# Performance work log

Measured on AMD Instinct MI355X. Metric: run time of the kernel, lower is better.

The kernel has to match this reference:

```python
import jax, jax.numpy as jnp
import numpy as np

HEADS = 8
HIDDEN = 512
SEQ = 1024
BATCH = 8
SCALE = 1.2
TOPK = round(0.05 * SEQ)  # 51, as in mode='stocastic'


def setup_inputs() -> dict:
    key = jax.random.key(0)
    ks = jax.random.split(key, 12)
    d = HIDDEN
    s = 0.02
    return {
        "Query_x": jax.random.normal(ks[0], (BATCH, SEQ, d), jnp.float32),
        "KeyandValue_x": jax.random.normal(ks[1], (BATCH, SEQ, d), jnp.float32),
        "Wq": jax.random.normal(ks[2], (d, d), jnp.float32) * s,
        "bq": jnp.zeros((d,), jnp.float32),
        "Wk": jax.random.normal(ks[3], (d, d), jnp.float32) * s,
        "bk": jnp.zeros((d,), jnp.float32),
        "Wv": jax.random.normal(ks[4], (d, d), jnp.float32) * s,
        "bv": jnp.zeros((d,), jnp.float32),
        "Wo": jax.random.normal(ks[5], (d, d), jnp.float32) * s,
        "bo": jnp.zeros((d,), jnp.float32),
        "randidx": jax.random.randint(ks[6], (round(0.1 * SEQ),), 0, SEQ, jnp.int32),
    }


def _split_heads(x, B, S):
    # torch: split last dim into heads chunks, cat along dim 0 -> [heads*B, S, dk]
    dk = HIDDEN // HEADS
    return x.reshape(B, S, HEADS, dk).transpose(2, 0, 1, 3).reshape(HEADS * B, S, dk)


def _merge_heads(x, B, S):
    dk = HIDDEN // HEADS
    return x.reshape(HEADS, B, S, dk).transpose(1, 2, 0, 3).reshape(B, S, HIDDEN)


def moderate_attention(a, randidx):
    # a: [N, S, L] softmaxed attention. Scale top-k + random columns by SCALE,
    # then renormalize rows. torch scatter_ writes a*SCALE gathered from the
    # pre-scatter tensor, so duplicate indices are idempotent -> boolean mask.
    N, S, L = a.shape
    _, idx = jax.lax.top_k(a, TOPK)                       # [N, S, k]
    rand_b = jnp.broadcast_to(randidx.astype(idx.dtype), (N, S, randidx.shape[0]))
    all_idx = jnp.concatenate([idx, rand_b], axis=-1)      # [N, S, k+r]
    n_ix = jnp.arange(N)[:, None, None]
    q_ix = jnp.arange(S)[None, :, None]
    sel = jnp.zeros(a.shape, bool).at[n_ix, q_ix, all_idx].set(True)
    a2 = jnp.where(sel, a * SCALE, a)
    return a2 / jnp.sum(a2, axis=-1, keepdims=True)


def reference(Query_x, KeyandValue_x, Wq, bq, Wk, bk, Wv, bv, Wo, bo, randidx):
    B, S, _ = Query_x.shape
    dk = HIDDEN // HEADS
    Q = _split_heads(Query_x @ Wq + bq, B, S)          # [H*B, S, dk]
    K = _split_heads(KeyandValue_x @ Wk + bk, B, S)
    V = _split_heads(KeyandValue_x @ Wv + bv, B, S)
    scores = jnp.einsum('nqd,nkd->nqk', Q, K) / jnp.sqrt(jnp.float32(dk))
    a = jax.nn.softmax(scores, axis=-1)
    a = moderate_attention(a, randidx)
    out = jnp.einsum('nqk,nkd->nqd', a, V)
    return _merge_heads(out, B, S) @ Wo + bo
```

## Files before the change

kernel.cpp:

```cpp
#include <hip/hip_runtime.h>
#include <stdint.h>

typedef unsigned short ushort_t;
typedef __bf16 bf16x8 __attribute__((ext_vector_type(8)));
typedef _Float16 f16x8v __attribute__((ext_vector_type(8)));
typedef __fp16 fp16x2 __attribute__((ext_vector_type(2)));
typedef float f32x4 __attribute__((ext_vector_type(4)));

#define SEQ   1024
#define DK    64
#define TOPK_N 51
#define RSCALE 1.2f

#define OFF_WT  0
#define OFF_Q   (4*512*512)
#define OFF_K   (OFF_Q  + 64*1024*64)
#define OFF_V   (OFF_K  + 64*1024*64)
#define OFF_QX  (OFF_V  + 64*1024*64)
#define OFF_KVX (OFF_QX + 8192*512)
#define OFF_MASK (OFF_KVX + 8192*512)
#define OFF_A   OFF_QX

static __device__ __forceinline__ ushort_t f2bf(float f){
  union { float f; unsigned u; } x; x.f = f;
  unsigned r = x.u + 0x7FFFu + ((x.u >> 16) & 1u);
  return (ushort_t)(r >> 16);
}
static __device__ __forceinline__ ushort_t f2h(float f){
  union { _Float16 h; ushort_t u; } x; x.h = (_Float16)f; return x.u;
}
static __device__ __forceinline__ float h2f(ushort_t u){
  union { ushort_t u; _Float16 h; } x; x.u = u; return (float)x.h;
}
static __device__ __forceinline__ unsigned pk2(float a, float b){
  union { fp16x2 h; unsigned u; } x;
  x.h = __builtin_amdgcn_cvt_pkrtz(a, b);
  return x.u;
}
static __device__ __forceinline__ bf16x8 frag16(const ushort_t* p){
  union { uint4 u; bf16x8 b; } x; x.u = *(const uint4*)p; return x.b;
}
static __device__ __forceinline__ f16x8v frag16h(const ushort_t* p){
  union { uint4 u; f16x8v h; } x; x.u = *(const uint4*)p; return x.h;
}
static __device__ __forceinline__ void gll16(const ushort_t* g, ushort_t* lds){
  __builtin_amdgcn_global_load_lds((const __attribute__((address_space(1))) unsigned*)g,
                                   (__attribute__((address_space(3))) unsigned*)lds,
                                   16, 0, 0);
}

__global__ __launch_bounds__(256) void prep_k(const float* qx, const float* kvx,
    const float* Wq, const float* Wk, const float* Wv, const float* Wo,
    const int* ridx, int nrand, ushort_t* ws){
  __shared__ ushort_t t[64][72];
  __shared__ unsigned wds[64];
  int bid = blockIdx.x, tid = threadIdx.x;

  if (bid < 4096){
    const float* src = (bid >= 2048) ? kvx : qx;
    ushort_t* dst = ws + ((bid >= 2048) ? OFF_KVX : OFF_QX);
    int i = ((bid & 2047)*256 + tid) * 8;
    float4 a = *(const float4*)(src + i);
    float4 b = *(const float4*)(src + i + 4);
    union { ushort_t s[8]; uint4 u; } p;
    p.s[0]=f2bf(a.x); p.s[1]=f2bf(a.y); p.s[2]=f2bf(a.z); p.s[3]=f2bf(a.w);
    p.s[4]=f2bf(b.x); p.s[5]=f2bf(b.y); p.s[6]=f2bf(b.z); p.s[7]=f2bf(b.w);
    *(uint4*)(dst + i) = p.u;
  } else if (bid < 4352){
    int rb = bid - 4096;
    int z = rb >> 6, rem = rb & 63;
    const float* W = z==0?Wq: z==1?Wk: z==2?Wv: Wo;
    ushort_t* O = ws + OFF_WT + (size_t)z*512*512;
    int kt = (rem >> 3)*64, nt = (rem & 7)*64;
    int r0 = tid>>3, c8 = (tid&7)*8;
    #pragma unroll
    for (int p=0;p<2;p++){
      int r = p*32 + r0;
      float4 a = *(const float4*)&W[(size_t)(kt+r)*512 + nt + c8];
      float4 b = *(const float4*)&W[(size_t)(kt+r)*512 + nt + c8 + 4];
      t[r][c8+0]=f2bf(a.x); t[r][c8+1]=f2bf(a.y); t[r][c8+2]=f2bf(a.z); t[r][c8+3]=f2bf(a.w);
      t[r][c8+4]=f2bf(b.x); t[r][c8+5]=f2bf(b.y); t[r][c8+6]=f2bf(b.z); t[r][c8+7]=f2bf(b.w);
    }
    __syncthreads();
    #pragma unroll
    for (int p=0;p<2;p++){
      int r = p*32 + r0;
      union { ushort_t s[8]; uint4 u; } tmp;
      #pragma unroll
      for (int j=0;j<8;j++) tmp.s[j] = t[c8+j][r];
      *(uint4*)&O[(size_t)(nt+r)*512 + kt + c8] = tmp.u;
    }
  } else {
    if (tid < 64) wds[tid] = 0;
    __syncthreads();
    for (int i = tid; i < nrand; i += 256){
      int col = ridx[i];
      atomicOr(&wds[(col >> 3) & 63], 1u << (((col >> 9) << 3) | (col & 7)));
    }
    __syncthreads();
    if (tid < 64) (ws + OFF_MASK)[tid] = (ushort_t)wds[tid];
  }
}

__global__ __launch_bounds__(256) void gemm_k(ushort_t* ws, const float* bq, const float* bk,
    const float* bv, const float* bo, float* dout, int base_mode){
  int mode = base_mode + blockIdx.z;
  const ushort_t* X  = (mode==0)? ws+OFF_QX : (mode==3)? ws+OFF_A : ws+OFF_KVX;
  const ushort_t* WT = ws + OFF_WT + (size_t)mode*(512*512);
  const float* bias  = (mode==0)?bq:(mode==1)?bk:(mode==2)?bv:bo;
  ushort_t* out = (mode==0)? ws+OFF_Q : (mode==1)? ws+OFF_K : ws+OFF_V;

  __shared__ ushort_t sA[128*64];
  __shared__ ushort_t sB[128*64];
  int tid = threadIdx.x, lane = tid & 63, w = tid >> 6;
  int wm = w & 1, wn = w >> 1;
  int m0 = blockIdx.y * 128, n0 = blockIdx.x * 128;
  int r16 = lane & 15, quad = lane >> 4;
  int srow = lane >> 3, schunk = lane & 7;

  const f32x4 zero = {0.f,0.f,0.f,0.f};
  f32x4 acc[4][4];
  #pragma unroll
  for (int i=0;i<4;i++)
    #pragma unroll
    for (int j=0;j<4;j++) acc[i][j] = zero;

  for (int kb = 0; kb < 8; kb++){
    int k0 = kb*64;
    #pragma unroll
    for (int i=0;i<4;i++){
      int rb = w*32 + i*8;
      int gch = schunk ^ srow;
      gll16(X  + (size_t)(m0+rb+srow)*512 + k0 + gch*8, sA + rb*64);
      gll16(WT + (size_t)(n0+rb+srow)*512 + k0 + gch*8, sB + rb*64);
    }
    __syncthreads();
    #pragma unroll
    for (int t=0;t<2;t++){
      bf16x8 aF[4], bF[4];
      #pragma unroll
      for (int i=0;i<4;i++){
        int row = wm*64 + i*16 + r16;
        aF[i] = frag16(sA + row*64 + ((t*4 + quad) ^ (row & 7))*8);
      }
      #pragma unroll
      for (int j=0;j<4;j++){
        int row = wn*64 + j*16 + r16;
        bF[j] = frag16(sB + row*64 + ((t*4 + quad) ^ (row & 7))*8);
      }
      #pragma unroll
      for (int i=0;i<4;i++)
        #pragma unroll
        for (int j=0;j<4;j++)
          acc[i][j] = __builtin_amdgcn_mfma_f32_16x16x32_bf16(aF[i], bF[j], acc[i][j], 0,0,0);
    }
    __syncthreads();
  }

  #pragma unroll
  for (int i=0;i<4;i++){
    int rowbase = m0 + wm*64 + i*16 + quad*4;
    #pragma unroll
    for (int j=0;j<4;j++){
      int col = n0 + wn*64 + j*16 + r16;
      float bsv = bias[col];
      if (mode == 3){
        #pragma unroll
        for (int r=0;r<4;r++)
          dout[(size_t)(rowbase+r)*512 + col] = acc[i][j][r] + bsv;
      } else if (mode == 2){
        int b = rowbase >> 10, s = rowbase & 1023;
        int h = col >> 6, d = col & 63;
        int nh = h*8 + b;
        int sb2 = s >> 2;
        union { ushort_t sh[4]; uint2 u2; } pk;
        #pragma unroll
        for (int r=0;r<4;r++) pk.sh[r] = f2h(acc[i][j][r] + bsv);
        *(uint2*)&out[ (((size_t)nh*256 + sb2)*64 + d)*4 ] = pk.u2;
      } else if (mode == 1){
        int b = rowbase >> 10;
        int h = col >> 6, d = col & 63;
        int nh = h*8 + b;
        size_t base = (size_t)nh*65536 + (size_t)(d>>3)*8192 + (d&7);
        #pragma unroll
        for (int r=0;r<4;r++){
          int s = (rowbase + r) & 1023;
          out[ base + (size_t)s*8 ] = f2bf(acc[i][j][r] + bsv);
        }
      } else {
        int h = col >> 6, d = col & 63;
        #pragma unroll
        for (int r=0;r<4;r++){
          int row = rowbase + r;
          int b = row >> 10, s = row & 1023;
          int nh = h*8 + b;
          out[ ((size_t)nh*1024 + s)*64 + d ] = f2bf((acc[i][j][r] + bsv)*0.125f);
        }
      }
    }
  }
}

__global__ __launch_bounds__(256, 5) void attn_k(const ushort_t* ws_q, const ushort_t* ws_k,
     const ushort_t* ws_v, const ushort_t* maskp, ushort_t* attn){
  __shared__ __align__(16) ushort_t sS[16*1024];

  int tid = threadIdx.x, lane = tid&63, w = tid>>6;
  int r16 = lane&15, quad = lane>>4;
  int gid = blockIdx.x;
  int n  = (gid & 7)*8 + ((gid >> 3) >> 6);
  int q0 = ((gid >> 3) & 63) * 16;
  const ushort_t* Qn = ws_q + (size_t)n*SEQ*DK;
  const ushort_t* Kn = ws_k + (size_t)n*SEQ*DK;
  const ushort_t* Vb = ws_v + (size_t)n*SEQ*DK;

  unsigned rmask = (unsigned)maskp[lane];

  bf16x8 aQ[2];
  #pragma unroll
  for (int t=0;t<2;t++)
    aQ[t] = frag16(Qn + (size_t)(q0 + r16)*64 + t*32 + quad*8);

  const f32x4 zero = {0.f,0.f,0.f,0.f};

  #pragma unroll
  for (int half=0; half<2; half++){
    f32x4 acc[8];
    #pragma unroll
    for (int i=0;i<8;i++) acc[i] = zero;
    #pragma unroll
    for (int grp=0; grp<2; grp++){
      int c = half*2 + grp;
      bf16x8 bF[8];
      #pragma unroll
      for (int u=0;u<4;u++){
        int key = c*256 + w*64 + u*16 + r16;
        bF[u*2+0] = frag16(Kn + ((size_t)(quad    )*1024 + key)*8);
        bF[u*2+1] = frag16(Kn + ((size_t)(4 + quad)*1024 + key)*8);
      }
      #pragma unroll
      for (int u=0;u<4;u++){
        int t8 = grp*4 + u;
        acc[t8] = __builtin_amdgcn_mfma_f32_16x16x32_bf16(aQ[0], bF[u*2+0], acc[t8], 0,0,0);
        acc[t8] = __builtin_amdgcn_mfma_f32_16x16x32_bf16(aQ[1], bF[u*2+1], acc[t8], 0,0,0);
      }
    }
    #pragma unroll
    for (int grp=0; grp<2; grp++)
      #pragma unroll
      for (int u=0;u<4;u++){
        int c = half*2 + grp;
        int col = c*256 + w*64 + u*16 + r16;
        int c0 = col>>3, c7 = col&7;
        #pragma unroll
        for (int r=0;r<4;r++){
          int row = quad*4 + r;
          sS[row*1024 + ((c0 ^ (row&7))*8) + c7] = f2h(acc[grp*4+u][r]);
        }
      }
  }
  __syncthreads();

  float v[4][16];
  float vmax[4];
  #pragma unroll
  for (int r=0;r<4;r++){
    int row = w*4 + r, rs = row & 7;
    const ushort_t* bp = sS + row*1024 + ((lane ^ rs) * 8);
    uint4 lo4 = *(const uint4*)bp;
    uint4 hi4 = *(const uint4*)(bp + 512);
    unsigned wl[8] = {lo4.x, lo4.y, lo4.z, lo4.w, hi4.x, hi4.y, hi4.z, hi4.w};
    float m = -3.0e38f;
    #pragma unroll
    for (int k=0;k<8;k++){
      float a = h2f((ushort_t)(wl[k] & 0xffffu));
      float b = h2f((ushort_t)(wl[k] >> 16));
      v[r][2*k] = a; v[r][2*k+1] = b;
      m = fmaxf(m, fmaxf(a, b));
    }
    vmax[r] = m;
  }
  #pragma unroll
  for (int off=32; off>=1; off>>=1)
    #pragma unroll
    for (int r=0;r<4;r++) vmax[r] = fmaxf(vmax[r], __shfl_xor(vmax[r], off));

  float blo[4], bhi[4];
  #pragma unroll
  for (int r=0;r<4;r++){ bhi[r] = vmax[r]; blo[r] = vmax[r] - 8.0f; }
  #pragma unroll 1
  for (int it=0; it<12; it++){
    #pragma unroll
    for (int r=0;r<4;r++){
      float mid = 0.5f*(blo[r]+bhi[r]);
      int cnt = 0;
      #pragma unroll
      for (int j=0;j<16;j++)
        cnt += __popcll(__ballot(v[r][j] >= mid));
      bool ge = (cnt >= TOPK_N);
      blo[r] = ge ? mid : blo[r];
      bhi[r] = ge ? bhi[r] : mid;
    }
  }
  float ls[4];
  #pragma unroll
  for (int r=0;r<4;r++){
    float thr = blo[r], s = 0.f;
    #pragma unroll
    for (int j=0;j<16;j++){
      bool sel = (v[r][j] >= thr) || ((rmask >> j) & 1u);
      float e = __expf(v[r][j] - vmax[r]);
      e = sel ? e*RSCALE : e;
      v[r][j] = e; s += e;
    }
    ls[r] = s;
  }
  #pragma unroll
  for (int off=32; off>=1; off>>=1)
    #pragma unroll
    for (int r=0;r<4;r++) ls[r] += __shfl_xor(ls[r], off);
  #pragma unroll
  for (int r=0;r<4;r++){
    int row = w*4 + r, rs = row & 7;
    float rinv = 1.0f / ls[r];
    ushort_t* bp = sS + row*1024 + ((lane ^ rs) * 8);
    uint4 o0, o1;
    o0.x = pk2(v[r][0]*rinv,  v[r][1]*rinv);
    o0.y = pk2(v[r][2]*rinv,  v[r][3]*rinv);
    o0.z = pk2(v[r][4]*rinv,  v[r][5]*rinv);
    o0.w = pk2(v[r][6]*rinv,  v[r][7]*rinv);
    o1.x = pk2(v[r][8]*rinv,  v[r][9]*rinv);
    o1.y = pk2(v[r][10]*rinv, v[r][11]*rinv);
    o1.z = pk2(v[r][12]*rinv, v[r][13]*rinv);
    o1.w = pk2(v[r][14]*rinv, v[r][15]*rinv);
    *(uint4*)bp = o0;
    *(uint4*)(bp + 512) = o1;
  }
  __syncthreads();

  f32x4 oa0 = zero, oa1 = zero;
  int dd = w*16 + r16;
  #pragma unroll
  for (int kb2=0; kb2<8; kb2++){
    f16x8v bV[4], aP[4];
    #pragma unroll
    for (int u=0;u<4;u++){
      int g8 = (kb2*4 + u)*4 + quad;
      size_t vb = ((size_t)(g8*2)*64 + dd)*4;
      uint2 l0 = *(const uint2*)&Vb[vb];
      uint2 l1 = *(const uint2*)&Vb[vb + 256];
      union { uint4 u4; f16x8v h; } bb;
      bb.u4 = make_uint4(l0.x, l0.y, l1.x, l1.y);
      bV[u] = bb.h;
      aP[u] = frag16h(sS + r16*1024 + (g8 ^ (r16&7))*8);
    }
    #pragma unroll
    for (int u=0;u<4;u++){
      if (u&1) oa1 = __builtin_amdgcn_mfma_f32_16x16x32_f16(aP[u], bV[u], oa1, 0,0,0);
      else     oa0 = __builtin_amdgcn_mfma_f32_16x16x32_f16(aP[u], bV[u], oa0, 0,0,0);
    }
  }
  f32x4 oacc = oa0 + oa1;

  int h = n >> 3, b = n & 7;
  #pragma unroll
  for (int r=0;r<4;r++){
    int s = q0 + quad*4 + r;
    attn[ ((size_t)(b*1024 + s))*512 + h*64 + w*16 + r16 ] = f2bf(oacc[r]);
  }
}

extern "C" void kernel_launch(void* const* d_in, const int* in_sizes, int n_in,
                              void* d_out, int out_size, void* d_ws, size_t ws_size,
                              hipStream_t stream){
  const float* Qx  = (const float*)d_in[0];
  const float* KVx = (const float*)d_in[1];
  const float* Wq  = (const float*)d_in[2];
  const float* bq  = (const float*)d_in[3];
  const float* Wk  = (const float*)d_in[4];
  const float* bk  = (const float*)d_in[5];
  const float* Wv  = (const float*)d_in[6];
  const float* bv  = (const float*)d_in[7];
  const float* Wo  = (const float*)d_in[8];
  const float* bo  = (const float*)d_in[9];
  const int* ridx  = (const int*)d_in[10];
  int nrand = in_sizes[10];
  ushort_t* ws = (ushort_t*)d_ws;
  float* dout = (float*)d_out;

  prep_k<<<4353, 256, 0, stream>>>(Qx, KVx, Wq, Wk, Wv, Wo, ridx, nrand, ws);
  gemm_k<<<dim3(4,64,3), 256, 0, stream>>>(ws, bq, bk, bv, bo, dout, 0);
  attn_k<<<4096, 256, 0, stream>>>(ws+OFF_Q, ws+OFF_K, ws+OFF_V, ws+OFF_MASK, ws+OFF_A);
  gemm_k<<<dim3(4,64,1), 256, 0, stream>>>(ws, bq, bk, bv, bo, dout, 3);
}
```

Before: 248.1 us.

## Rework attention kernel: transposed QK MFMA, packed stores, V layout, exp2 scaling

Swaps the MFMA operand order in QK^T so each lane holds four consecutive keys of one query row, allowing packed 8-byte fp16 stores into the swizzled LDS score tile instead of scalar stores. V is now written in an 8-wide interleaved layout so each PV fragment is one 16-byte load. The softmax folds the 1.2 top-k/random scale into an exp2 bias via fma, and the top-k bisection window and iteration count are reduced. It also adds s_setprio around the MFMA blocks and lowers the occupancy hint from 5 to 4. The narrower bisection window (max-4) risks a wrong threshold for rows whose 51st-largest score sits further below the max.

```diff
diff --git a/kernel.cpp b/kernel.cpp
--- a/kernel.cpp
+++ b/kernel.cpp
@@ -11,6 +11,8 @@
 #define DK    64
 #define TOPK_N 51
 #define RSCALE 1.2f
+#define LOG2E    1.44269504089f
+#define LOG2_12  0.26303440583f
 
 #define OFF_WT  0
 #define OFF_Q   (4*512*512)
@@ -36,6 +38,9 @@
   union { fp16x2 h; unsigned u; } x;
   x.h = __builtin_amdgcn_cvt_pkrtz(a, b);
   return x.u;
+}
+static __device__ __forceinline__ unsigned pkrne(float a, float b){
+  return (unsigned)f2h(a) | ((unsigned)f2h(b) << 16);
 }
 static __device__ __forceinline__ bf16x8 frag16(const ushort_t* p){
   union { uint4 u; bf16x8 b; } x; x.u = *(const uint4*)p; return x.b;
@@ -172,11 +177,10 @@
         int b = rowbase >> 10, s = rowbase & 1023;
         int h = col >> 6, d = col & 63;
         int nh = h*8 + b;
-        int sb2 = s >> 2;
         union { ushort_t sh[4]; uint2 u2; } pk;
         #pragma unroll
         for (int r=0;r<4;r++) pk.sh[r] = f2h(acc[i][j][r] + bsv);
-        *(uint2*)&out[ (((size_t)nh*256 + sb2)*64 + d)*4 ] = pk.u2;
+        *(uint2*)&out[ (((size_t)nh*128 + (s>>3))*64 + d)*8 + (s&4) ] = pk.u2;
       } else if (mode == 1){
         int b = rowbase >> 10;
         int h = col >> 6, d = col & 63;
@@ -201,7 +205,7 @@
   }
 }
 
-__global__ __launch_bounds__(256, 5) void attn_k(const ushort_t* ws_q, const ushort_t* ws_k,
+__global__ __launch_bounds__(256, 4) void attn_k(const ushort_t* ws_q, const ushort_t* ws_k,
      const ushort_t* ws_v, const ushort_t* maskp, ushort_t* attn){
   __shared__ __align__(16) ushort_t sS[16*1024];
 
@@ -238,25 +242,26 @@
         bF[u*2+0] = frag16(Kn + ((size_t)(quad    )*1024 + key)*8);
         bF[u*2+1] = frag16(Kn + ((size_t)(4 + quad)*1024 + key)*8);
       }
+      __builtin_amdgcn_s_setprio(1);
       #pragma unroll
       for (int u=0;u<4;u++){
         int t8 = grp*4 + u;
-        acc[t8] = __builtin_amdgcn_mfma_f32_16x16x32_bf16(aQ[0], bF[u*2+0], acc[t8], 0,0,0);
-        acc[t8] = __builtin_amdgcn_mfma_f32_16x16x32_bf16(aQ[1], bF[u*2+1], acc[t8], 0,0,0);
-      }
-    }
+        acc[t8] = __builtin_amdgcn_mfma_f32_16x16x32_bf16(bF[u*2+0], aQ[0], acc[t8], 0,0,0);
+        acc[t8] = __builtin_amdgcn_mfma_f32_16x16x32_bf16(bF[u*2+1], aQ[1], acc[t8], 0,0,0);
+      }
+      __builtin_amdgcn_s_setprio(0);
+    }
+    int rs = r16 & 7;
     #pragma unroll
     for (int grp=0; grp<2; grp++)
       #pragma unroll
       for (int u=0;u<4;u++){
-        int c = half*2 + grp;
-        int col = c*256 + w*64 + u*16 + r16;
-        int c0 = col>>3, c7 = col&7;
-        #pragma unroll
-        for (int r=0;r<4;r++){
-          int row = quad*4 + r;
-          sS[row*1024 + ((c0 ^ (row&7))*8) + c7] = f2h(acc[grp*4+u][r]);
-        }
+        int kb = (half*2+grp)*256 + w*64 + u*16 + quad*4;
+        f32x4 a = acc[grp*4+u];
+        uint2 o;
+        o.x = pkrne(a[0], a[1]);
+        o.y = pkrne(a[2], a[3]);
+        *(uint2*)(sS + r16*1024 + (((kb>>3) ^ rs) << 3) + (kb & 4)) = o;
       }
   }
   __syncthreads();
@@ -281,15 +286,21 @@
     vmax[r] = m;
   }
   #pragma unroll
+  for (int r=0;r<4;r++)
+    #pragma unroll
+    for (int j=0;j<16;j++)
+      asm volatile("" : "+v"(v[r][j]));
+
+  #pragma unroll
   for (int off=32; off>=1; off>>=1)
     #pragma unroll
     for (int r=0;r<4;r++) vmax[r] = fmaxf(vmax[r], __shfl_xor(vmax[r], off));
 
   float blo[4], bhi[4];
   #pragma unroll
-  for (int r=0;r<4;r++){ bhi[r] = vmax[r]; blo[r] = vmax[r] - 8.0f; }
+  for (int r=0;r<4;r++){ bhi[r] = vmax[r]; blo[r] = vmax[r] - 4.0f; }
   #pragma unroll 1
-  for (int it=0; it<12; it++){
+  for (int it=0; it<11; it++){
     #pragma unroll
     for (int r=0;r<4;r++){
       float mid = 0.5f*(blo[r]+bhi[r]);
@@ -302,15 +313,21 @@
       bhi[r] = ge ? bhi[r] : mid;
     }
   }
+  float fb[16];
+  #pragma unroll
+  for (int j=0;j<16;j++) fb[j] = ((rmask >> j) & 1u) ? LOG2_12 : 0.0f;
+  float sC = LOG2_12;
+  asm volatile("" : "+v"(sC));
+
   float ls[4];
   #pragma unroll
   for (int r=0;r<4;r++){
     float thr = blo[r], s = 0.f;
     #pragma unroll
     for (int j=0;j<16;j++){
-      bool sel = (v[r][j] >= thr) || ((rmask >> j) & 1u);
-      float e = __expf(v[r][j] - vmax[r]);
-      e = sel ? e*RSCALE : e;
+      float tb = (v[r][j] >= thr) ? sC : fb[j];
+      float e = __builtin_amdgcn_exp2f(
+                  __builtin_fmaf(v[r][j] - vmax[r], LOG2E, tb));
       v[r][j] = e; s += e;
     }
     ls[r] = s;
@@ -346,19 +363,16 @@
     #pragma unroll
     for (int u=0;u<4;u++){
       int g8 = (kb2*4 + u)*4 + quad;
-      size_t vb = ((size_t)(g8*2)*64 + dd)*4;
-      uint2 l0 = *(const uint2*)&Vb[vb];
-      uint2 l1 = *(const uint2*)&Vb[vb + 256];
-      union { uint4 u4; f16x8v h; } bb;
-      bb.u4 = make_uint4(l0.x, l0.y, l1.x, l1.y);
-      bV[u] = bb.h;
-      aP[u] = frag16h(sS + r16*1024 + (g8 ^ (r16&7))*8);
-    }
+      bV[u] = frag16h(Vb + ((size_t)g8*64 + dd)*8);
+      aP[u] = frag16h(sS + r16*1024 + ((g8 ^ (r16&7))*8));
+    }
+    __builtin_amdgcn_s_setprio(1);
     #pragma unroll
     for (int u=0;u<4;u++){
       if (u&1) oa1 = __builtin_amdgcn_mfma_f32_16x16x32_f16(aP[u], bV[u], oa1, 0,0,0);
       else     oa0 = __builtin_amdgcn_mfma_f32_16x16x32_f16(aP[u], bV[u], oa0, 0,0,0);
     }
+    __builtin_amdgcn_s_setprio(0);
   }
   f32x4 oacc = oa0 + oa1;
 
```

Result: faster. 234.9 us (-5.3%).
